# Kernel tuning notes

Hardware: AMD Instinct MI355X
Metric: run time of the kernel (lower is better)

## Reference

```python
import jax, jax.numpy as jnp
import numpy as np

B, N, D = 4, 512, 128
NEG = -1e9


def setup_inputs() -> dict:
    key = jax.random.key(0)
    ks = jax.random.split(key, 11)
    s = 1.0 / np.sqrt(D)
    inp = {
        "q": jax.random.normal(ks[0], (B, N, D), jnp.float32),
        "k": jax.random.normal(ks[1], (B, N, D), jnp.float32),
        "v": jax.random.normal(ks[2], (B, N, D), jnp.float32),
        "mask": jnp.ones((B, N), jnp.int32),
        # nn.Linear params: weight [out,in], bias [out]
        "Wq": jax.random.uniform(ks[3], (D, D), jnp.float32, -s, s),
        "bq": jax.random.uniform(ks[4], (D,), jnp.float32, -s, s),
        "Wk": jax.random.uniform(ks[5], (D, D), jnp.float32, -s, s),
        "bk": jax.random.uniform(ks[6], (D,), jnp.float32, -s, s),
        "Wv": jax.random.uniform(ks[7], (D, D), jnp.float32, -s, s),
        "bv": jax.random.uniform(ks[8], (D,), jnp.float32, -s, s),
        "Wo": jax.random.uniform(ks[9], (D, D), jnp.float32, -s, s),
        "bo": jax.random.uniform(ks[10], (D,), jnp.float32, -s, s),
    }
    return inp


def reference(q, k, v, mask, Wq, bq, Wk, bk, Wv, bv, Wo, bo):
    # linear projections (torch Linear: x @ W.T + b)
    qp = jnp.einsum('bnd,ed->bne', q, Wq) + bq
    kp = jnp.einsum('bnd,ed->bne', k, Wk) + bk
    vp = jnp.einsum('bnd,ed->bne', v, Wv) + bv
    # outer-product attention: scores [b, n, m, d]
    scores = jnp.einsum('bnd,bmd->bnmd', qp, kp)
    # mask [b, n] -> [b, n, 1, 1], fill masked positions with -1e9
    scores = jnp.where(mask[:, :, None, None] == 0, NEG, scores)
    # per-channel softmax over m (axis=2); dropout is a no-op at inference
    scores = jax.nn.softmax(scores, axis=2)
    out = jnp.einsum('bnmd,bmd->bnd', scores, vp)
    return jnp.einsum('bnd,ed->bne', out, Wo) + bo
```

## Files before the change

### kernel.cpp

```cpp
#include <hip/hip_runtime.h>

#define BB 4
#define NN 512
#define DD 128

static constexpr float LOG2E = 1.4426950408889634f;
#define EXP2F(x) __builtin_amdgcn_exp2f(x)

__global__ __launch_bounds__(256) void wtrans_kernel(
    const float* __restrict__ Wq, const float* __restrict__ Wk,
    const float* __restrict__ Wv, const float* __restrict__ Wo,
    float* __restrict__ WTp)
{
    const int l = blockIdx.x * 256 + threadIdx.x;
    const int t = l >> 14;
    const int e = (l >> 7) & (DD - 1);
    const int j = l & (DD - 1);
    const float* W = (t == 0) ? Wq : (t == 1) ? Wk : (t == 2) ? Wv : Wo;
    WTp[(t << 14) + (j >> 2) * (DD * 4) + e * 4 + (j & 3)] = W[e * DD + j];
}

__global__ __launch_bounds__(512) void proj_kernel(
    const float* __restrict__ q, const float* __restrict__ k,
    const float* __restrict__ v, const float* __restrict__ WTp,
    const float* __restrict__ bq, const float* __restrict__ bk,
    const float* __restrict__ bv,
    float* __restrict__ qpT, float* __restrict__ kpT, float* __restrict__ vpT)
{
    const int t   = blockIdx.y;
    const int e   = threadIdx.x & (DD - 1);
    const int sub = threadIdx.x >> 7;
    const int g0  = blockIdx.x * 8 + sub * 2;

    const float*  x    = (t == 0) ? q   : (t == 1) ? k   : v;
    const float4* wt4  = (const float4*)(WTp + (t << 14));
    const float*  bias = (t == 0) ? bq  : (t == 1) ? bk  : bv;
    float*        outp = (t == 0) ? qpT : (t == 1) ? kpT : vpT;
    const float scale  = (t == 0) ? LOG2E : 1.0f;

    const float4* x0 = (const float4*)(x + g0 * DD);
    const float4* x1 = (const float4*)(x + (g0 + 1) * DD);

    float a0 = 0.f, a1 = 0.f;
    #pragma unroll 8
    for (int j4 = 0; j4 < DD / 4; ++j4) {
        const float4 w  = wt4[j4 * DD + e];
        const float4 r0 = x0[j4];
        const float4 r1 = x1[j4];
        a0 = fmaf(r0.x, w.x, fmaf(r0.y, w.y, fmaf(r0.z, w.z, fmaf(r0.w, w.w, a0))));
        a1 = fmaf(r1.x, w.x, fmaf(r1.y, w.y, fmaf(r1.z, w.z, fmaf(r1.w, w.w, a1))));
    }

    const float be = bias[e];
    {
        const int b = g0 >> 9, n = g0 & (NN - 1);
        outp[(b * DD + e) * NN + n] = (a0 + be) * scale;
    }
    {
        const int g = g0 + 1;
        const int b = g >> 9, n = g & (NN - 1);
        outp[(b * DD + e) * NN + n] = (a1 + be) * scale;
    }
}

__global__ __launch_bounds__(512) void attn_kernel(
    const float* __restrict__ qpT, const float* __restrict__ kpT,
    const float* __restrict__ vpT, const int* __restrict__ mask,
    float* __restrict__ att)
{
    __shared__ float sk[NN];
    __shared__ float sv[NN];

    const int bd = blockIdx.x;
    const int b  = bd >> 7;
    const int d  = bd & (DD - 1);
    const int n  = threadIdx.x;

    sk[n] = kpT[bd * NN + n];
    sv[n] = vpT[bd * NN + n];

    float qv = qpT[bd * NN + n];
    if (mask[b * NN + n] == 0) qv = 0.f;
    __syncthreads();

    const float4* k4p = (const float4*)sk;
    const float4* v4p = (const float4*)sv;

    float n0 = 0.f, n1 = 0.f, n2 = 0.f, n3 = 0.f;
    float d0 = 0.f, d1 = 0.f;
    #pragma unroll 8
    for (int m4 = 0; m4 < NN / 4; ++m4) {
        const float4 k4 = k4p[m4];
        const float4 v4 = v4p[m4];
        const float p0 = EXP2F(qv * k4.x);
        const float p1 = EXP2F(qv * k4.y);
        const float p2 = EXP2F(qv * k4.z);
        const float p3 = EXP2F(qv * k4.w);
        n0 = fmaf(p0, v4.x, n0);
        n1 = fmaf(p1, v4.y, n1);
        n2 = fmaf(p2, v4.z, n2);
        n3 = fmaf(p3, v4.w, n3);
        d0 += p0 + p1;
        d1 += p2 + p3;
    }

    att[(b * NN + n) * DD + d] = ((n0 + n1) + (n2 + n3)) / (d0 + d1);
}

__global__ __launch_bounds__(512) void outproj_kernel(
    const float* __restrict__ att, const float* __restrict__ WTp,
    const float* __restrict__ bo, float* __restrict__ out)
{
    const int e   = threadIdx.x & (DD - 1);
    const int sub = threadIdx.x >> 7;
    const int g   = blockIdx.x * 4 + sub;

    const float4* wt4 = (const float4*)(WTp + (3 << 14));
    const float4* xr  = (const float4*)(att + g * DD);

    float acc = 0.f;
    #pragma unroll 8
    for (int j4 = 0; j4 < DD / 4; ++j4) {
        const float4 w = wt4[j4 * DD + e];
        const float4 a = xr[j4];
        acc = fmaf(a.x, w.x, fmaf(a.y, w.y, fmaf(a.z, w.z, fmaf(a.w, w.w, acc))));
    }

    out[g * DD + e] = acc + bo[e];
}

extern "C" void kernel_launch(void* const* d_in, const int* in_sizes, int n_in,
                              void* d_out, int out_size, void* d_ws, size_t ws_size,
                              hipStream_t stream)
{
    const float* q    = (const float*)d_in[0];
    const float* k    = (const float*)d_in[1];
    const float* v    = (const float*)d_in[2];
    const int*   mask = (const int*)  d_in[3];
    const float* Wq   = (const float*)d_in[4];
    const float* bq   = (const float*)d_in[5];
    const float* Wk   = (const float*)d_in[6];
    const float* bk   = (const float*)d_in[7];
    const float* Wv   = (const float*)d_in[8];
    const float* bv   = (const float*)d_in[9];
    const float* Wo   = (const float*)d_in[10];
    const float* bo   = (const float*)d_in[11];
    float* out = (float*)d_out;

    float* ws  = (float*)d_ws;
    float* qpT = ws;
    float* kpT = ws + 1 * BB * DD * NN;
    float* vpT = ws + 2 * BB * DD * NN;
    float* att = ws + 3 * BB * DD * NN;
    float* WTp = ws + 4 * BB * DD * NN;

    wtrans_kernel<<<4 * DD * DD / 256, 256, 0, stream>>>(Wq, Wk, Wv, Wo, WTp);

    dim3 pgrid(BB * NN / 8, 3);
    proj_kernel<<<pgrid, 512, 0, stream>>>(q, k, v, WTp, bq, bk, bv, qpT, kpT, vpT);

    attn_kernel<<<BB * DD, 512, 0, stream>>>(qpT, kpT, vpT, mask, att);

    outproj_kernel<<<BB * NN / 4, 512, 0, stream>>>(att, WTp, bo, out);
}
```

Baseline: 130.7 us.

## Register-block attention over four queries per thread and split keys across groups

Each attention thread now handles four query rows and a quarter of the key range, so every float4 of K and V read from shared memory is reused across four exp2/FMA chains. Partial numerators and denominators are reduced through shared memory after a second barrier. Mask handling moves into the projection kernel, which zeroes masked query values there. This trades extra registers, shared memory and a reduction step for fewer LDS reads per exponential.

```diff
diff --git a/kernel.cpp b/kernel.cpp
--- a/kernel.cpp
+++ b/kernel.cpp
@@ -24,7 +24,7 @@
     const float* __restrict__ q, const float* __restrict__ k,
     const float* __restrict__ v, const float* __restrict__ WTp,
     const float* __restrict__ bq, const float* __restrict__ bk,
-    const float* __restrict__ bv,
+    const float* __restrict__ bv, const int* __restrict__ mask,
     float* __restrict__ qpT, float* __restrict__ kpT, float* __restrict__ vpT)
 {
     const int t   = blockIdx.y;
@@ -36,7 +36,6 @@
     const float4* wt4  = (const float4*)(WTp + (t << 14));
     const float*  bias = (t == 0) ? bq  : (t == 1) ? bk  : bv;
     float*        outp = (t == 0) ? qpT : (t == 1) ? kpT : vpT;
-    const float scale  = (t == 0) ? LOG2E : 1.0f;
 
     const float4* x0 = (const float4*)(x + g0 * DD);
     const float4* x1 = (const float4*)(x + (g0 + 1) * DD);
@@ -52,59 +51,74 @@
     }
 
     const float be = bias[e];
-    {
-        const int b = g0 >> 9, n = g0 & (NN - 1);
-        outp[(b * DD + e) * NN + n] = (a0 + be) * scale;
-    }
-    {
-        const int g = g0 + 1;
+    #pragma unroll
+    for (int r = 0; r < 2; ++r) {
+        const int g = g0 + r;
         const int b = g >> 9, n = g & (NN - 1);
-        outp[(b * DD + e) * NN + n] = (a1 + be) * scale;
+        float val = (r == 0 ? a0 : a1) + be;
+        if (t == 0) val = (mask[g] != 0) ? val * LOG2E : 0.f;
+        outp[(b * DD + e) * NN + n] = val;
     }
 }
 
 __global__ __launch_bounds__(512) void attn_kernel(
     const float* __restrict__ qpT, const float* __restrict__ kpT,
-    const float* __restrict__ vpT, const int* __restrict__ mask,
-    float* __restrict__ att)
+    const float* __restrict__ vpT, float* __restrict__ att)
 {
     __shared__ float sk[NN];
     __shared__ float sv[NN];
+    __shared__ float pn[4][NN];
+    __shared__ float pd[4][NN];
 
-    const int bd = blockIdx.x;
-    const int b  = bd >> 7;
-    const int d  = bd & (DD - 1);
-    const int n  = threadIdx.x;
+    const int bd  = blockIdx.x;
+    const int b   = bd >> 7;
+    const int d   = bd & (DD - 1);
+    const int tid = threadIdx.x;
+    const int h   = tid >> 7;
+    const int i   = tid & 127;
 
-    sk[n] = kpT[bd * NN + n];
-    sv[n] = vpT[bd * NN + n];
+    sk[tid] = kpT[bd * NN + tid];
+    sv[tid] = vpT[bd * NN + tid];
 
-    float qv = qpT[bd * NN + n];
-    if (mask[b * NN + n] == 0) qv = 0.f;
+    float qv[4];
+    #pragma unroll
+    for (int j = 0; j < 4; ++j)
+        qv[j] = qpT[bd * NN + i + j * 128];
     __syncthreads();
 
-    const float4* k4p = (const float4*)sk;
-    const float4* v4p = (const float4*)sv;
+    const float4* kc = (const float4*)sk;
+    const float4* vc = (const float4*)sv;
 
-    float n0 = 0.f, n1 = 0.f, n2 = 0.f, n3 = 0.f;
-    float d0 = 0.f, d1 = 0.f;
-    #pragma unroll 8
-    for (int m4 = 0; m4 < NN / 4; ++m4) {
-        const float4 k4 = k4p[m4];
-        const float4 v4 = v4p[m4];
-        const float p0 = EXP2F(qv * k4.x);
-        const float p1 = EXP2F(qv * k4.y);
-        const float p2 = EXP2F(qv * k4.z);
-        const float p3 = EXP2F(qv * k4.w);
-        n0 = fmaf(p0, v4.x, n0);
-        n1 = fmaf(p1, v4.y, n1);
-        n2 = fmaf(p2, v4.z, n2);
-        n3 = fmaf(p3, v4.w, n3);
-        d0 += p0 + p1;
-        d1 += p2 + p3;
+    float na[4] = {0.f, 0.f, 0.f, 0.f}, nb[4] = {0.f, 0.f, 0.f, 0.f};
+    float da[4] = {0.f, 0.f, 0.f, 0.f}, db[4] = {0.f, 0.f, 0.f, 0.f};
+
+    const int m4lo = h * 32;
+    #pragma unroll 4
+    for (int m4 = m4lo; m4 < m4lo + 32; ++m4) {
+        const float4 k4 = kc[m4];
+        const float4 v4 = vc[m4];
+        #pragma unroll
+        for (int j = 0; j < 4; ++j) {
+            const float p0 = EXP2F(qv[j] * k4.x);
+            const float p1 = EXP2F(qv[j] * k4.y);
+            const float p2 = EXP2F(qv[j] * k4.z);
+            const float p3 = EXP2F(qv[j] * k4.w);
+            na[j] = fmaf(p0, v4.x, na[j]); nb[j] = fmaf(p1, v4.y, nb[j]);
+            na[j] = fmaf(p2, v4.z, na[j]); nb[j] = fmaf(p3, v4.w, nb[j]);
+            da[j] += p0 + p2;              db[j] += p1 + p3;
+        }
     }
 
-    att[(b * NN + n) * DD + d] = ((n0 + n1) + (n2 + n3)) / (d0 + d1);
+    #pragma unroll
+    for (int j = 0; j < 4; ++j) {
+        pn[h][i + j * 128] = na[j] + nb[j];
+        pd[h][i + j * 128] = da[j] + db[j];
+    }
+    __syncthreads();
+
+    const float num = pn[0][tid] + pn[1][tid] + pn[2][tid] + pn[3][tid];
+    const float den = pd[0][tid] + pd[1][tid] + pd[2][tid] + pd[3][tid];
+    att[(b * NN + tid) * DD + d] = num / den;
 }
 
 __global__ __launch_bounds__(512) void outproj_kernel(
@@ -157,9 +171,10 @@
     wtrans_kernel<<<4 * DD * DD / 256, 256, 0, stream>>>(Wq, Wk, Wv, Wo, WTp);
 
     dim3 pgrid(BB * NN / 8, 3);
-    proj_kernel<<<pgrid, 512, 0, stream>>>(q, k, v, WTp, bq, bk, bv, qpT, kpT, vpT);
+    proj_kernel<<<pgrid, 512, 0, stream>>>(q, k, v, WTp, bq, bk, bv, mask,
+                                           qpT, kpT, vpT);
 
-    attn_kernel<<<BB * DD, 512, 0, stream>>>(qpT, kpT, vpT, mask, att);
+    attn_kernel<<<BB * DD, 512, 0, stream>>>(qpT, kpT, vpT, att);
 
     outproj_kernel<<<BB * NN / 4, 512, 0, stream>>>(att, WTp, bo, out);
 }
```

After: 127.1 us. 2.8% less time.
